# Kernel tuning notes

Hardware: AMD Instinct MI355X
Metric: run time of the kernel (lower is better)

## Reference

```python
import jax, jax.numpy as jnp
import numpy as np

N_SCALES = 4
WINDOW = 64
REDUCTION = 4
EPS = 5e-05


def conv3x3_reflect(x, w):
    # reflect pad 1 then VALID 3x3 conv (no bias), NCHW/OIHW
    xp = jnp.pad(x, ((0, 0), (0, 0), (1, 1), (1, 1)), mode='reflect')
    return jax.lax.conv_general_dilated(
        xp, w, window_strides=(1, 1), padding='VALID',
        dimension_numbers=('NCHW', 'OIHW', 'NCHW'))


def add_adjacent_clusters(x):
    # x: (N, u, k, w, e); concat rolled-back and rolled-forward clusters on window axis
    x_back = jnp.roll(x, 1, axis=2)
    x_fwd = jnp.roll(x, -1, axis=2)
    return jnp.concatenate([x, x_back, x_fwd], axis=3)


def setup_inputs() -> dict:
    key = jax.random.key(0)
    ks = jax.random.split(key, 6)
    N, Cin, H, W = 2, 200, 128, 128
    inp = {
        'input': jax.random.normal(ks[0], (N, Cin, H, W), dtype=jnp.float32),
        'semantic_label': jax.random.randint(ks[1], (N, N_SCALES, H, W), 0, 32, dtype=jnp.int32),
        'Wx': jax.random.normal(ks[2], (Cin // REDUCTION, Cin, 3, 3), dtype=jnp.float32) * 0.02,
        'Wy': jax.random.normal(ks[3], (Cin, Cin, 1, 1), dtype=jnp.float32) * 0.02,
        'Wout': jax.random.normal(ks[4], (Cin, Cin * N_SCALES, 1, 1), dtype=jnp.float32) * 0.02,
        'bout': jax.random.normal(ks[5], (Cin,), dtype=jnp.float32) * 0.02,
    }
    return inp


def reference(input, semantic_label, Wx, Wy, Wout, bout):
    N, Cin, H, W = input.shape
    L = H * W
    C = Cin // REDUCTION  # 50

    # embeddings: (N, L, C) and (N, L, C*reduction)
    x_embed = conv3x3_reflect(input, Wx).reshape(N, C, L).transpose(0, 2, 1)
    y_embed = jnp.einsum('nchw,oc->nohw', input, Wy[:, :, 0, 0]).reshape(N, Cin, L).transpose(0, 2, 1)

    # semantic prior embed: per-scale offset of 100, flatten to (N, n_scales*L)
    offsets = (jnp.arange(N_SCALES, dtype=semantic_label.dtype) * 100)[None, :, None]
    sl = (semantic_label.reshape(N, N_SCALES, L) + offsets).reshape(N, -1)

    indices = jnp.argsort(sl, axis=-1)          # (N, n_scales*L)
    undo_sort = jnp.argsort(indices, axis=-1)
    mod_indices = indices % L

    x_sorted = jnp.take_along_axis(x_embed, mod_indices[:, :, None], axis=1)  # (N, 4L, C)
    y_sorted = jnp.take_along_axis(y_embed, mod_indices[:, :, None], axis=1)  # (N, 4L, 4C)

    # L chosen divisible by window_size -> padding == 0
    assert L % WINDOW == 0
    K = L // WINDOW
    x_cl = x_sorted.reshape(N, N_SCALES, K, WINDOW, C)
    y_cl = y_sorted.reshape(N, N_SCALES, K, WINDOW, C * REDUCTION)

    # F.normalize(p=2, dim=-1, eps=5e-5): x / max(||x||, eps)
    norm = jnp.linalg.norm(x_cl, axis=-1, keepdims=True)
    x_match = x_cl / jnp.maximum(norm, EPS)
    x_match = add_adjacent_clusters(x_match)    # (N, u, K, 3*W, C)
    y_adj = add_adjacent_clusters(y_cl)         # (N, u, K, 3*W, 4C)

    raw_weight = jnp.einsum('bukie,bukje->bukij', x_cl, x_match)  # (N,u,K,W,3W)
    weight = jax.nn.softmax(raw_weight, axis=-1)  # exp(raw - logsumexp)
    out = jnp.einsum('bukij,bukje->bukie', weight, y_adj)          # (N,u,K,W,4C)

    out = out.reshape(N, N_SCALES * L, C * REDUCTION)
    out = jnp.take_along_axis(out, undo_sort[:, :, None], axis=1)  # unsort
    out = out.reshape(N, N_SCALES, L, C * REDUCTION)
    out = out.transpose(0, 1, 3, 2).reshape(N, N_SCALES * C * REDUCTION, H, W)

    # 1x1 conv_out with bias + residual
    out = jnp.einsum('nchw,oc->nohw', out, Wout[:, :, 0, 0]) + bout[None, :, None, None]
    return out + input
```

## Files before the change

kernel.cpp:

```cpp
#include <hip/hip_runtime.h>
#include <hip/hip_bf16.h>
#include <math.h>

#define L      16384
#define CIN    200
#define CE     50
#define NS     4
#define KCL    256
#define WIN    64
#define NKEY   192

__global__ __launch_bounds__(256) void k_conv3(const float* __restrict__ in,
                                               const float* __restrict__ Wx,
                                               float* __restrict__ xe) {
  const int ocg  = blockIdx.x;
  const int tile = blockIdx.y;
  const int n    = blockIdx.z;
  const int th = tile >> 3, tw = tile & 7;
  const int ty = threadIdx.x >> 4, tx = threadIdx.x & 15;
  const int oc0 = ocg * 10;
  const int tid = threadIdx.x;

  __shared__ __align__(16) float patch[4 * 18 * 20];

  const float* inN = in + (size_t)n * CIN * L;
  const float* wB  = Wx + (size_t)oc0 * CIN * 9;

  int goff[6], loff[6];
#pragma unroll
  for (int j = 0; j < 6; ++j) {
    int idx = tid + j * 256;
    if (idx < 1296) {
      int ic = idx / 324, rem = idx % 324;
      int r = rem / 18, c = rem % 18;
      int gh = th * 16 + r - 1, gw = tw * 16 + c - 1;
      gh = gh < 0 ? -gh : (gh > 127 ? 254 - gh : gh);
      gw = gw < 0 ? -gw : (gw > 127 ? 254 - gw : gw);
      goff[j] = ic * L + gh * 128 + gw;
      loff[j] = ic * 360 + r * 20 + c;
    } else {
      goff[j] = -1;
      loff[j] = 0;
    }
  }

  float acc[10];
#pragma unroll
  for (int o = 0; o < 10; ++o) acc[o] = 0.f;

  float pf[6];
#pragma unroll
  for (int j = 0; j < 6; ++j) pf[j] = (goff[j] >= 0) ? inN[goff[j]] : 0.f;

  for (int s = 0; s < 50; ++s) {
    __syncthreads();
#pragma unroll
    for (int j = 0; j < 6; ++j)
      if (goff[j] >= 0) patch[loff[j]] = pf[j];
    __syncthreads();
    if (s < 49) {
      const float* src = inN + (size_t)(s + 1) * 4 * L;
#pragma unroll
      for (int j = 0; j < 6; ++j) pf[j] = (goff[j] >= 0) ? src[goff[j]] : 0.f;
    }

    float p[4][9];
#pragma unroll
    for (int icc = 0; icc < 4; ++icc) {
      const float* pb = &patch[icc * 360 + ty * 20 + tx];
#pragma unroll
      for (int dr = 0; dr < 3; ++dr)
#pragma unroll
        for (int dc = 0; dc < 3; ++dc)
          p[icc][dr * 3 + dc] = pb[dr * 20 + dc];
    }
    const float* wS = wB + (size_t)(4 * s) * 9;
#pragma unroll
    for (int o = 0; o < 10; ++o) {
      const float* wO = wS + (size_t)o * CIN * 9;
#pragma unroll
      for (int icc = 0; icc < 4; ++icc)
#pragma unroll
        for (int q = 0; q < 9; ++q)
          acc[o] = fmaf(p[icc][q], wO[icc * 9 + q], acc[o]);
    }
  }

  const int l = (th * 16 + ty) * 128 + (tw * 16 + tx);
  float* xrow = xe + ((size_t)n * L + l) * CE + oc0;
#pragma unroll
  for (int o = 0; o < 5; ++o)
    *(float2*)&xrow[o * 2] = make_float2(acc[o * 2], acc[o * 2 + 1]);
}

__global__ __launch_bounds__(256) void k_wy(const float* __restrict__ in,
                                            const float* __restrict__ Wy,
                                            float* __restrict__ ye) {
  const int n  = blockIdx.y;
  const int l0 = blockIdx.x * 64;
  __shared__ __align__(16) float At[20][64];
  __shared__ __align__(16) float Wt[20][208];
  const int pg = threadIdx.x >> 4, og = threadIdx.x & 15;

  float acc[4][13];
#pragma unroll
  for (int p = 0; p < 4; ++p)
#pragma unroll
    for (int j = 0; j < 13; ++j) acc[p][j] = 0.f;

  for (int idx = threadIdx.x; idx < 20 * 8; idx += 256)
    Wt[idx >> 3][200 + (idx & 7)] = 0.f;

  const float* inN = in + (size_t)n * CIN * L + l0;
  for (int c0 = 0; c0 < CIN; c0 += 20) {
    __syncthreads();
    for (int idx = threadIdx.x; idx < 20 * 64; idx += 256) {
      int k = idx >> 6, p = idx & 63;
      At[k][p] = inN[(size_t)(c0 + k) * L + p];
    }
    for (int idx = threadIdx.x; idx < 200 * 20; idx += 256) {
      int oc = idx / 20, k = idx % 20;
      Wt[k][oc] = Wy[(size_t)oc * CIN + c0 + k];
    }
    __syncthreads();
#pragma unroll
    for (int k = 0; k < 20; ++k) {
      float4 av = *(const float4*)&At[k][pg * 4];
      float a[4] = {av.x, av.y, av.z, av.w};
      float b[13];
#pragma unroll
      for (int j = 0; j < 13; ++j) b[j] = Wt[k][og * 13 + j];
#pragma unroll
      for (int p = 0; p < 4; ++p)
#pragma unroll
        for (int j = 0; j < 13; ++j) acc[p][j] = fmaf(a[p], b[j], acc[p][j]);
    }
  }
#pragma unroll
  for (int p = 0; p < 4; ++p) {
    int l = l0 + pg * 4 + p;
    float* yrow = ye + ((size_t)n * L + l) * CIN;
#pragma unroll
    for (int j = 0; j < 13; ++j) {
      int oc = og * 13 + j;
      if (oc < CIN) yrow[oc] = acc[p][j];
    }
  }
}

__global__ __launch_bounds__(256) void k_hist(const int* __restrict__ sl,
                                              int* __restrict__ hist) {
  const int blk = blockIdx.x;
  const int n = blk >> 7, ch = blk & 127;
  __shared__ int h[128];
  if (threadIdx.x < 128) h[threadIdx.x] = 0;
  __syncthreads();
#pragma unroll
  for (int it = 0; it < 2; ++it) {
    int pos = ch * 512 + it * 256 + threadIdx.x;
    int u = pos >> 14, l = pos & (L - 1);
    int lab = sl[((size_t)n * NS + u) * L + l] & 31;
    atomicAdd(&h[u * 32 + lab], 1);
  }
  __syncthreads();
  if (threadIdx.x < 128) hist[(blk << 7) + threadIdx.x] = h[threadIdx.x];
}

__global__ __launch_bounds__(128) void k_scan(const int* __restrict__ hist,
                                              int* __restrict__ offs) {
  const int n = blockIdx.x, b = threadIdx.x;
  __shared__ int tot[128];
  __shared__ int basebuf[128];
  int t = 0;
  for (int c = 0; c < 128; ++c) t += hist[(((size_t)n * 128 + c) << 7) + b];
  tot[b] = t;
  __syncthreads();
  if (b == 0) {
    int run = 0;
    for (int i = 0; i < 128; ++i) { basebuf[i] = run; run += tot[i]; }
  }
  __syncthreads();
  int run = basebuf[b];
  for (int c = 0; c < 128; ++c) {
    offs[(((size_t)n * 128 + c) << 7) + b] = run;
    run += hist[(((size_t)n * 128 + c) << 7) + b];
  }
}

__global__ __launch_bounds__(512) void k_scatter(const int* __restrict__ sl,
                                                 const int* __restrict__ offs,
                                                 int* __restrict__ perm) {
  const int blk = blockIdx.x;
  const int n = blk >> 7, ch = blk & 127;
  const int tid = threadIdx.x, wv = tid >> 6, lane = tid & 63;
  __shared__ int wh[8][128];
  for (int idx = tid; idx < 1024; idx += 512) ((int*)wh)[idx] = 0;
  __syncthreads();
  const int pos = ch * 512 + tid;
  const int u = pos >> 14, l = pos & (L - 1);
  const int b = u * 32 + (sl[((size_t)n * NS + u) * L + l] & 31);
  atomicAdd(&wh[wv][b], 1);
  int lr = 0;
  for (int s = 0; s < 64; ++s) {
    int ob = __shfl(b, s);
    lr += (s < lane && ob == b) ? 1 : 0;
  }
  __syncthreads();
  if (tid < 128) {
    int run = 0;
#pragma unroll
    for (int w = 0; w < 8; ++w) { int v = wh[w][tid]; wh[w][tid] = run; run += v; }
  }
  __syncthreads();
  const int rank = offs[(blk << 7) + b] + wh[wv][b] + lr;
  perm[(size_t)n * (NS * L) + rank] = pos;
}

#define PT_P  66
#define QS_P  68
#define KS_P  196
#define YT_P  228

__global__ __launch_bounds__(512) void k_attn(const float* __restrict__ xe,
                                              const float* __restrict__ ye,
                                              const int* __restrict__ perm,
                                              float* __restrict__ attnO) {
  const int kcl = blockIdx.x;
  const int u   = blockIdx.y;
  const int n   = blockIdx.z;
  const int tid = threadIdx.x;

  __shared__ __align__(16) char smraw[112384];
  float* Pt   = (float*)smraw;
  float* Qst  = (float*)(smraw + 50688);
  float* Kst  = (float*)(smraw + 50688 + 13600);
  float* Yt   = (float*)(smraw + 50688);
  int*   lidx = (int*)(smraw + 50688 + 58368);
  float* rmax = (float*)(smraw + 50688 + 58368 + 768);
  float* rsum = (float*)(smraw + 50688 + 58368 + 1024);
  float* red  = (float*)(smraw + 50688 + 58368 + 1280);

  if (tid < NKEY) {
    int kj = tid < 64 ? kcl
           : (tid < 128 ? ((kcl + KCL - 1) & (KCL - 1)) : ((kcl + 1) & (KCL - 1)));
    int p = (u << 14) + (kj << 6) + (tid & 63);
    lidx[tid] = perm[(size_t)n * (NS * L) + p] & (L - 1);
  }
  __syncthreads();

  for (int idx = tid; idx < NKEY * CE; idx += 512) {
    int j = idx / CE, c = idx % CE;
    float v = xe[((size_t)n * L + lidx[j]) * CE + c];
    Kst[c * KS_P + j] = v;
    if (j < WIN) Qst[c * QS_P + j] = v;
  }
  __syncthreads();

  if (tid < NKEY) {
    float s = 0.f;
#pragma unroll
    for (int c = 0; c < CE; ++c) { float v = Kst[c * KS_P + tid]; s += v * v; }
    float inv = 1.f / fmaxf(sqrtf(s), 5e-5f);
#pragma unroll
    for (int c = 0; c < CE; ++c) Kst[c * KS_P + tid] *= inv;
  }
  __syncthreads();

  {
    const int ig = tid >> 5, jg = tid & 31;
    const int i0 = ig * 4, j0 = jg * 6;
    float s[4][6];
#pragma unroll
    for (int a = 0; a < 4; ++a)
#pragma unroll
      for (int b = 0; b < 6; ++b) s[a][b] = 0.f;
    for (int c = 0; c < CE; ++c) {
      float4 qv = *(const float4*)&Qst[c * QS_P + i0];
      float q[4] = {qv.x, qv.y, qv.z, qv.w};
      float kv[6];
#pragma unroll
      for (int b = 0; b < 6; ++b) kv[b] = Kst[c * KS_P + j0 + b];
#pragma unroll
      for (int a = 0; a < 4; ++a)
#pragma unroll
        for (int b = 0; b < 6; ++b) s[a][b] = fmaf(q[a], kv[b], s[a][b]);
    }
#pragma unroll
    for (int b = 0; b < 6; ++b)
#pragma unroll
      for (int a = 0; a < 4; ++a) Pt[(j0 + b) * PT_P + (i0 + a)] = s[a][b];
  }
  __syncthreads();

  {
    const int i = tid >> 3, q = tid & 7;
    float m = -1e30f;
#pragma unroll
    for (int jj = 0; jj < 24; ++jj) m = fmaxf(m, Pt[(q * 24 + jj) * PT_P + i]);
    red[i * 8 + q] = m;
    __syncthreads();
    if (q == 0) {
      float mm = red[i * 8];
#pragma unroll
      for (int t = 1; t < 8; ++t) mm = fmaxf(mm, red[i * 8 + t]);
      rmax[i] = mm;
    }
    __syncthreads();
    float mm = rmax[i];
    float ss = 0.f;
#pragma unroll
    for (int jj = 0; jj < 24; ++jj) {
      float v = expf(Pt[(q * 24 + jj) * PT_P + i] - mm);
      Pt[(q * 24 + jj) * PT_P + i] = v;
      ss += v;
    }
    red[i * 8 + q] = ss;
    __syncthreads();
    if (q == 0) {
      float s2 = 0.f;
#pragma unroll
      for (int t = 0; t < 8; ++t) s2 += red[i * 8 + t];
      rsum[i] = 1.f / s2;
    }
    __syncthreads();
    float inv = rsum[i];
#pragma unroll
    for (int jj = 0; jj < 24; ++jj) Pt[(q * 24 + jj) * PT_P + i] *= inv;
  }

  const int i = tid & 63, q = tid >> 6;
  float acc[28];
#pragma unroll
  for (int e = 0; e < 28; ++e) acc[e] = 0.f;

  for (int T = 0; T < 3; ++T) {
    __syncthreads();
    for (int idx = tid; idx < 64 * 57; idx += 512) {
      int jj = idx / 57, f = idx % 57;
      float4 v = make_float4(0.f, 0.f, 0.f, 0.f);
      if (f < 50)
        v = *(const float4*)&ye[((size_t)n * L + lidx[T * 64 + jj]) * CIN + f * 4];
      *(float4*)&Yt[jj * YT_P + f * 4] = v;
    }
    __syncthreads();
#pragma unroll 4
    for (int jj = 0; jj < 64; ++jj) {
      float p = Pt[(T * 64 + jj) * PT_P + i];
      const float* yrow = &Yt[jj * YT_P + q * 28];
#pragma unroll
      for (int f = 0; f < 7; ++f) {
        float4 yv = *(const float4*)&yrow[f * 4];
        acc[f * 4 + 0] = fmaf(p, yv.x, acc[f * 4 + 0]);
        acc[f * 4 + 1] = fmaf(p, yv.y, acc[f * 4 + 1]);
        acc[f * 4 + 2] = fmaf(p, yv.z, acc[f * 4 + 2]);
        acc[f * 4 + 3] = fmaf(p, yv.w, acc[f * 4 + 3]);
      }
    }
  }

  {
    const int l  = lidx[i];
    const int e0 = q * 28;
    float* orow = attnO + (((size_t)(n * NS + u) * L) + l) * CIN + e0;
    const int nf = (e0 + 28 <= CIN) ? 7 : (CIN - e0) / 4;
#pragma unroll
    for (int f = 0; f < 7; ++f)
      if (f < nf)
        *(float4*)&orow[f * 4] =
            make_float4(acc[f * 4], acc[f * 4 + 1], acc[f * 4 + 2], acc[f * 4 + 3]);
  }
}

__global__ __launch_bounds__(256) void k_wout(const float* __restrict__ attnO,
                                              const float* __restrict__ Wo,
                                              const float* __restrict__ bo,
                                              const float* __restrict__ in,
                                              float* __restrict__ out) {
  const int n  = blockIdx.y;
  const int l0 = blockIdx.x * 64;
  __shared__ __align__(16) char sm[44160];
  float* At = (float*)sm;
  float* Wt = (float*)(sm + 10880);
  const int pg = threadIdx.x >> 4, og = threadIdx.x & 15;
  const int tid = threadIdx.x;

  float acc[4][13];
#pragma unroll
  for (int p = 0; p < 4; ++p)
#pragma unroll
    for (int j = 0; j < 13; ++j) acc[p][j] = 0.f;

  for (int idx = tid; idx < 40 * 8; idx += 256)
    Wt[(idx >> 3) * 208 + 200 + (idx & 7)] = 0.f;

  for (int c0 = 0; c0 < 800; c0 += 40) {
    const int u = c0 / 200, e0 = c0 % 200;
    __syncthreads();
    for (int idx = tid; idx < 64 * 40; idx += 256) {
      int p = idx / 40, kk = idx % 40;
      At[kk * 68 + p] = attnO[(((size_t)(n * NS + u) * L) + l0 + p) * CIN + e0 + kk];
    }
    for (int idx = tid; idx < 200 * 40; idx += 256) {
      int oc = idx / 40, kk = idx % 40;
      Wt[kk * 208 + oc] = Wo[(size_t)oc * 800 + c0 + kk];
    }
    __syncthreads();
#pragma unroll 8
    for (int kk = 0; kk < 40; ++kk) {
      float4 av = *(const float4*)&At[kk * 68 + pg * 4];
      float a[4] = {av.x, av.y, av.z, av.w};
      float b[13];
#pragma unroll
      for (int j = 0; j < 13; ++j) b[j] = Wt[kk * 208 + og * 13 + j];
#pragma unroll
      for (int p = 0; p < 4; ++p)
#pragma unroll
        for (int j = 0; j < 13; ++j) acc[p][j] = fmaf(a[p], b[j], acc[p][j]);
    }
  }
  __syncthreads();

  float* Ot = (float*)sm;
  for (int r = 0; r < 2; ++r) {
    const int ocb = r * 104;
    const int width = (r == 0) ? 104 : 96;
#pragma unroll
    for (int p = 0; p < 4; ++p)
#pragma unroll
      for (int j = 0; j < 13; ++j) {
        int oc = og * 13 + j;
        if (oc >= ocb && oc < ocb + width)
          Ot[(oc - ocb) * 64 + pg * 4 + p] = acc[p][j];
      }
    __syncthreads();
    for (int idx = tid; idx < width * 64; idx += 256) {
      int oc2 = idx >> 6, p = idx & 63;
      size_t o = ((size_t)n * CIN + ocb + oc2) * L + l0 + p;
      out[o] = Ot[oc2 * 64 + p] + bo[ocb + oc2] + in[o];
    }
    __syncthreads();
  }
}

extern "C" void kernel_launch(void* const* d_in, const int* in_sizes, int n_in,
                              void* d_out, int out_size, void* d_ws, size_t ws_size,
                              hipStream_t stream) {
  const float* in = (const float*)d_in[0];
  const int*   sl = (const int*)d_in[1];
  const float* Wx = (const float*)d_in[2];
  const float* Wy = (const float*)d_in[3];
  const float* Wo = (const float*)d_in[4];
  const float* bo = (const float*)d_in[5];
  float* out = (float*)d_out;

  float* xe   = (float*)d_ws;
  float* ye   = xe + (size_t)2 * L * CE;
  float* attn = ye + (size_t)2 * L * CIN;
  int*   perm = (int*)(attn + (size_t)2 * NS * L * CIN);
  int*   hist = perm + (size_t)2 * NS * L;
  int*   offs = hist + (size_t)2 * 128 * 128;

  k_conv3  <<<dim3(5, 64, 2),  256, 0, stream>>>(in, Wx, xe);
  k_wy     <<<dim3(256, 2),    256, 0, stream>>>(in, Wy, ye);
  k_hist   <<<256,             256, 0, stream>>>(sl, hist);
  k_scan   <<<2,               128, 0, stream>>>(hist, offs);
  k_scatter<<<256,             512, 0, stream>>>(sl, offs, perm);
  k_attn   <<<dim3(256, 4, 2), 512, 0, stream>>>(xe, ye, perm, attn);
  k_wout   <<<dim3(256, 2),    256, 0, stream>>>(attn, Wo, bo, in, out);
}
```

Before: 1.207 ms.

## Restructure attention kernel into online-softmax over key tiles with direct global Y reads

```diff
diff --git a/kernel.cpp b/kernel.cpp
--- a/kernel.cpp
+++ b/kernel.cpp
@@ -216,10 +216,9 @@
   perm[(size_t)n * (NS * L) + rank] = pos;
 }
 
-#define PT_P  66
+#define PT_P  65
 #define QS_P  68
-#define KS_P  196
-#define YT_P  228
+#define KS_P  68
 
 __global__ __launch_bounds__(512) void k_attn(const float* __restrict__ xe,
                                               const float* __restrict__ ye,
@@ -230,144 +229,139 @@
   const int n   = blockIdx.z;
   const int tid = threadIdx.x;
 
-  __shared__ __align__(16) char smraw[112384];
-  float* Pt   = (float*)smraw;
-  float* Qst  = (float*)(smraw + 50688);
-  float* Kst  = (float*)(smraw + 50688 + 13600);
-  float* Yt   = (float*)(smraw + 50688);
-  int*   lidx = (int*)(smraw + 50688 + 58368);
-  float* rmax = (float*)(smraw + 50688 + 58368 + 768);
-  float* rsum = (float*)(smraw + 50688 + 58368 + 1024);
-  float* red  = (float*)(smraw + 50688 + 58368 + 1280);
+  __shared__ __align__(16) float Qst[CE * QS_P];
+  __shared__ __align__(16) float Kst[CE * KS_P];
+  __shared__ __align__(16) float Pt[WIN * PT_P];
+  __shared__ int   lidxS[NKEY];
+  __shared__ float invn[WIN];
+  __shared__ float rmaxS[WIN];
+  __shared__ float rsumS[WIN];
+  __shared__ float facS[WIN];
 
   if (tid < NKEY) {
     int kj = tid < 64 ? kcl
            : (tid < 128 ? ((kcl + KCL - 1) & (KCL - 1)) : ((kcl + 1) & (KCL - 1)));
     int p = (u << 14) + (kj << 6) + (tid & 63);
-    lidx[tid] = perm[(size_t)n * (NS * L) + p] & (L - 1);
-  }
-  __syncthreads();
-
-  for (int idx = tid; idx < NKEY * CE; idx += 512) {
+    lidxS[tid] = perm[(size_t)n * (NS * L) + p] & (L - 1);
+  }
+  if (tid < WIN) { rmaxS[tid] = -1e30f; rsumS[tid] = 0.f; }
+  __syncthreads();
+
+  for (int idx = tid; idx < WIN * CE; idx += 512) {
     int j = idx / CE, c = idx % CE;
-    float v = xe[((size_t)n * L + lidx[j]) * CE + c];
-    Kst[c * KS_P + j] = v;
-    if (j < WIN) Qst[c * QS_P + j] = v;
-  }
-  __syncthreads();
-
-  if (tid < NKEY) {
-    float s = 0.f;
-#pragma unroll
-    for (int c = 0; c < CE; ++c) { float v = Kst[c * KS_P + tid]; s += v * v; }
-    float inv = 1.f / fmaxf(sqrtf(s), 5e-5f);
-#pragma unroll
-    for (int c = 0; c < CE; ++c) Kst[c * KS_P + tid] *= inv;
-  }
-  __syncthreads();
+    Qst[c * QS_P + j] = xe[((size_t)n * L + lidxS[j]) * CE + c];
+  }
+
+  const int i_sm = tid >> 3, q_sm = tid & 7;
+  const int ig = tid >> 5, jg = tid & 31;
+  const int li = tid & 63, wq = tid >> 6;
+  const int nf = (wq == 7) ? 1 : 7;
+
+  float acc[28];
+#pragma unroll
+  for (int e = 0; e < 28; ++e) acc[e] = 0.f;
+
+  for (int T = 0; T < 3; ++T) {
+    const int jb = T * 64;
+    __syncthreads();
+    for (int idx = tid; idx < WIN * CE; idx += 512) {
+      int j = idx / CE, c = idx % CE;
+      Kst[c * KS_P + j] = xe[((size_t)n * L + lidxS[jb + j]) * CE + c];
+    }
+    __syncthreads();
+
+    {
+      float s = 0.f;
+      for (int c = q_sm; c < CE; c += 8) {
+        float v = Kst[c * KS_P + i_sm];
+        s = fmaf(v, v, s);
+      }
+      s += __shfl_xor(s, 1); s += __shfl_xor(s, 2); s += __shfl_xor(s, 4);
+      if (q_sm == 0) invn[i_sm] = 1.f / fmaxf(sqrtf(s), 5e-5f);
+    }
+    __syncthreads();
+
+    {
+      float s00 = 0.f, s01 = 0.f, s10 = 0.f, s11 = 0.f, s20 = 0.f, s21 = 0.f,
+            s30 = 0.f, s31 = 0.f;
+      for (int c = 0; c < CE; ++c) {
+        float4 qv = *(const float4*)&Qst[c * QS_P + ig * 4];
+        float2 kv = *(const float2*)&Kst[c * KS_P + jg * 2];
+        s00 = fmaf(qv.x, kv.x, s00); s01 = fmaf(qv.x, kv.y, s01);
+        s10 = fmaf(qv.y, kv.x, s10); s11 = fmaf(qv.y, kv.y, s11);
+        s20 = fmaf(qv.z, kv.x, s20); s21 = fmaf(qv.z, kv.y, s21);
+        s30 = fmaf(qv.w, kv.x, s30); s31 = fmaf(qv.w, kv.y, s31);
+      }
+      float inv0 = invn[jg * 2], inv1 = invn[jg * 2 + 1];
+      float* p0 = &Pt[(jg * 2 + 0) * PT_P + ig * 4];
+      float* p1 = &Pt[(jg * 2 + 1) * PT_P + ig * 4];
+      p0[0] = s00 * inv0; p0[1] = s10 * inv0; p0[2] = s20 * inv0; p0[3] = s30 * inv0;
+      p1[0] = s01 * inv1; p1[1] = s11 * inv1; p1[2] = s21 * inv1; p1[3] = s31 * inv1;
+    }
+    __syncthreads();
+
+    {
+      float p[8];
+      float tm = -1e30f;
+#pragma unroll
+      for (int k = 0; k < 8; ++k) {
+        p[k] = Pt[(q_sm * 8 + k) * PT_P + i_sm];
+        tm = fmaxf(tm, p[k]);
+      }
+      tm = fmaxf(tm, __shfl_xor(tm, 1));
+      tm = fmaxf(tm, __shfl_xor(tm, 2));
+      tm = fmaxf(tm, __shfl_xor(tm, 4));
+      float mo = rmaxS[i_sm];
+      float nm = fmaxf(mo, tm);
+      float fc = __expf(mo - nm);
+      float ts = 0.f;
+#pragma unroll
+      for (int k = 0; k < 8; ++k) {
+        float v = __expf(p[k] - nm);
+        Pt[(q_sm * 8 + k) * PT_P + i_sm] = v;
+        ts += v;
+      }
+      ts += __shfl_xor(ts, 1); ts += __shfl_xor(ts, 2); ts += __shfl_xor(ts, 4);
+      if (q_sm == 0) {
+        rmaxS[i_sm] = nm;
+        rsumS[i_sm] = rsumS[i_sm] * fc + ts;
+        facS[i_sm]  = fc;
+      }
+    }
+    __syncthreads();
+
+    {
+      float fc = facS[li];
+#pragma unroll
+      for (int e = 0; e < 28; ++e) acc[e] *= fc;
+      const float* yeN = ye + (size_t)n * L * CIN + wq * 28;
+#pragma unroll 4
+      for (int jj = 0; jj < WIN; ++jj) {
+        float p = Pt[jj * PT_P + li];
+        const float* yrow = yeN + (size_t)lidxS[jb + jj] * CIN;
+#pragma unroll
+        for (int f = 0; f < 7; ++f) {
+          if (f < nf) {
+            float4 yv = *(const float4*)&yrow[f * 4];
+            acc[f * 4 + 0] = fmaf(p, yv.x, acc[f * 4 + 0]);
+            acc[f * 4 + 1] = fmaf(p, yv.y, acc[f * 4 + 1]);
+            acc[f * 4 + 2] = fmaf(p, yv.z, acc[f * 4 + 2]);
+            acc[f * 4 + 3] = fmaf(p, yv.w, acc[f * 4 + 3]);
+          }
+        }
+      }
+    }
+  }
 
   {
-    const int ig = tid >> 5, jg = tid & 31;
-    const int i0 = ig * 4, j0 = jg * 6;
-    float s[4][6];
-#pragma unroll
-    for (int a = 0; a < 4; ++a)
-#pragma unroll
-      for (int b = 0; b < 6; ++b) s[a][b] = 0.f;
-    for (int c = 0; c < CE; ++c) {
-      float4 qv = *(const float4*)&Qst[c * QS_P + i0];
-      float q[4] = {qv.x, qv.y, qv.z, qv.w};
-      float kv[6];
-#pragma unroll
-      for (int b = 0; b < 6; ++b) kv[b] = Kst[c * KS_P + j0 + b];
-#pragma unroll
-      for (int a = 0; a < 4; ++a)
-#pragma unroll
-        for (int b = 0; b < 6; ++b) s[a][b] = fmaf(q[a], kv[b], s[a][b]);
-    }
-#pragma unroll
-    for (int b = 0; b < 6; ++b)
-#pragma unroll
-      for (int a = 0; a < 4; ++a) Pt[(j0 + b) * PT_P + (i0 + a)] = s[a][b];
-  }
-  __syncthreads();
-
-  {
-    const int i = tid >> 3, q = tid & 7;
-    float m = -1e30f;
-#pragma unroll
-    for (int jj = 0; jj < 24; ++jj) m = fmaxf(m, Pt[(q * 24 + jj) * PT_P + i]);
-    red[i * 8 + q] = m;
-    __syncthreads();
-    if (q == 0) {
-      float mm = red[i * 8];
-#pragma unroll
-      for (int t = 1; t < 8; ++t) mm = fmaxf(mm, red[i * 8 + t]);
-      rmax[i] = mm;
-    }
-    __syncthreads();
-    float mm = rmax[i];
-    float ss = 0.f;
-#pragma unroll
-    for (int jj = 0; jj < 24; ++jj) {
-      float v = expf(Pt[(q * 24 + jj) * PT_P + i] - mm);
-      Pt[(q * 24 + jj) * PT_P + i] = v;
-      ss += v;
-    }
-    red[i * 8 + q] = ss;
-    __syncthreads();
-    if (q == 0) {
-      float s2 = 0.f;
-#pragma unroll
-      for (int t = 0; t < 8; ++t) s2 += red[i * 8 + t];
-      rsum[i] = 1.f / s2;
-    }
-    __syncthreads();
-    float inv = rsum[i];
-#pragma unroll
-    for (int jj = 0; jj < 24; ++jj) Pt[(q * 24 + jj) * PT_P + i] *= inv;
-  }
-
-  const int i = tid & 63, q = tid >> 6;
-  float acc[28];
-#pragma unroll
-  for (int e = 0; e < 28; ++e) acc[e] = 0.f;
-
-  for (int T = 0; T < 3; ++T) {
-    __syncthreads();
-    for (int idx = tid; idx < 64 * 57; idx += 512) {
-      int jj = idx / 57, f = idx % 57;
-      float4 v = make_float4(0.f, 0.f, 0.f, 0.f);
-      if (f < 50)
-        v = *(const float4*)&ye[((size_t)n * L + lidx[T * 64 + jj]) * CIN + f * 4];
-      *(float4*)&Yt[jj * YT_P + f * 4] = v;
-    }
-    __syncthreads();
-#pragma unroll 4
-    for (int jj = 0; jj < 64; ++jj) {
-      float p = Pt[(T * 64 + jj) * PT_P + i];
-      const float* yrow = &Yt[jj * YT_P + q * 28];
-#pragma unroll
-      for (int f = 0; f < 7; ++f) {
-        float4 yv = *(const float4*)&yrow[f * 4];
-        acc[f * 4 + 0] = fmaf(p, yv.x, acc[f * 4 + 0]);
-        acc[f * 4 + 1] = fmaf(p, yv.y, acc[f * 4 + 1]);
-        acc[f * 4 + 2] = fmaf(p, yv.z, acc[f * 4 + 2]);
-        acc[f * 4 + 3] = fmaf(p, yv.w, acc[f * 4 + 3]);
-      }
-    }
-  }
-
-  {
-    const int l  = lidx[i];
-    const int e0 = q * 28;
-    float* orow = attnO + (((size_t)(n * NS + u) * L) + l) * CIN + e0;
-    const int nf = (e0 + 28 <= CIN) ? 7 : (CIN - e0) / 4;
+    float is = 1.f / rsumS[li];
+    const int l = lidxS[li];
+    float* orow = attnO + (((size_t)(n * NS + u) * L) + l) * CIN + wq * 28;
 #pragma unroll
     for (int f = 0; f < 7; ++f)
       if (f < nf)
-        *(float4*)&orow[f * 4] =
-            make_float4(acc[f * 4], acc[f * 4 + 1], acc[f * 4 + 2], acc[f * 4 + 3]);
+        *(float4*)&orow[f * 4] = make_float4(acc[f * 4] * is, acc[f * 4 + 1] * is,
+                                             acc[f * 4 + 2] * is, acc[f * 4 + 3] * is);
   }
 }
 
```

Measured after the change: 1.734 ms. 43.7% more time.
